# Kernel tuning notes

Hardware: AMD Instinct MI355X
Metric: run time of the kernel (lower is better)

Reference implementation:

```python
import jax, jax.numpy as jnp
import numpy as np

B, S, FEAT, HID, H = 8, 1024, 1024, 1024, 8
DH = HID // H  # head dim = 128
MASK_VAL = -128.0  # mask_val = -2**7 (soft additive mask, per original code)


def setup_inputs() -> dict:
    key = jax.random.key(0)
    ks = jax.random.split(key, 4)
    scale = 0.02
    return {
        "queries": jax.random.normal(ks[0], (B, S, FEAT), dtype=jnp.float32),
        "Wq": jax.random.normal(ks[1], (FEAT, HID), dtype=jnp.float32) * scale,
        "bq": jnp.zeros((HID,), dtype=jnp.float32),
        "Wk": jax.random.normal(ks[2], (FEAT, HID), dtype=jnp.float32) * scale,
        "bk": jnp.zeros((HID,), dtype=jnp.float32),
        "Wv": jax.random.normal(ks[3], (FEAT, HID), dtype=jnp.float32) * scale,
        "bv": jnp.zeros((HID,), dtype=jnp.float32),
    }


def reference(queries, Wq, bq, Wk, bk, Wv, bv):
    # Self-attention: keys = values = queries (torch forward defaults)
    q = queries @ Wq + bq  # [B,S,HID]
    k = queries @ Wk + bk
    v = queries @ Wv + bv
    # split heads: chunk along last dim == reshape (B,S,H,DH)
    qh = q.reshape(B, S, H, DH)
    kh = k.reshape(B, S, H, DH)
    vh = v.reshape(B, S, H, DH)
    # exp-scaled-dot score (non-standard: exp BEFORE mask/softmax)
    logits = jnp.einsum("bqhd,bkhd->bhqk", qh, kh) / np.float32(np.sqrt(DH))
    score = jnp.exp(logits)
    # soft additive causal mask: upper triangle (diag=1) gets -128
    mask = jnp.triu(jnp.full((S, S), MASK_VAL, dtype=score.dtype), k=1)
    att = jax.nn.softmax(score + mask, axis=-1)  # [B,H,S,S]
    ctx = jnp.einsum("bhqk,bkhd->bqhd", att, vh)  # [B,S,H,DH]
    # reverse heads: concat along last dim
    return ctx.reshape(B, S, HID)
```

## Files before the change

kernel.cpp:

```cpp
#include <hip/hip_runtime.h>


typedef __bf16 bf16x8 __attribute__((ext_vector_type(8)));
typedef float floatx4 __attribute__((ext_vector_type(4)));
typedef unsigned short u16;
typedef unsigned int u32;

#define RSCALE 0.08838834764831845f

__device__ __forceinline__ u16 f2b(float f) {
  union { float f; unsigned u; } v; v.f = f;
  return (u16)((v.u + 0x7FFFu + ((v.u >> 16) & 1u)) >> 16);
}

__device__ __forceinline__ void gld_lds16(const void* g, void* l) {
  __builtin_amdgcn_global_load_lds(
      (const __attribute__((address_space(1))) unsigned*)g,
      (__attribute__((address_space(3))) unsigned*)l, 16, 0, 0);
}

#define MFMA16(a, b, c) __builtin_amdgcn_mfma_f32_16x16x32_bf16(a, b, c, 0, 0, 0)

__device__ __forceinline__ void barrier_mem() {
  asm volatile("" ::: "memory");
  __builtin_amdgcn_s_barrier();
  asm volatile("" ::: "memory");
}
#define WAIT_LGKM0() asm volatile("s_waitcnt lgkmcnt(0)" ::: "memory")
#define WAIT_VM4()   asm volatile("s_waitcnt vmcnt(4)" ::: "memory")
#define WAIT_VM0()   asm volatile("s_waitcnt vmcnt(0)" ::: "memory")

__global__ __launch_bounds__(256) void prep_kernel(
    const float4* __restrict__ X, u16* __restrict__ Xb,
    const float* __restrict__ Wq, const float* __restrict__ Wk,
    const float* __restrict__ Wv, u16* __restrict__ Wtb) {
  if (blockIdx.x < 8192) {
    unsigned i = blockIdx.x * 256u + threadIdx.x;
    float4 v = X[i];
    ushort4 o;
    o.x = f2b(v.x); o.y = f2b(v.y); o.z = f2b(v.z); o.w = f2b(v.w);
    *reinterpret_cast<ushort4*>(Xb + 4u * i) = o;
  } else {
    const int bid = blockIdx.x - 8192;
    const int mat = bid >> 10;
    const int bx = bid & 31, by = (bid >> 5) & 31;
    const float* W = (mat == 0) ? Wq : (mat == 1) ? Wk : Wv;
    u16* Wt = Wtb + (size_t)mat * (1024u * 1024u);
    __shared__ u16 tile[32][33];
    const int x = threadIdx.x & 31, y = threadIdx.x >> 5;
    const int kt = bx * 32, nt = by * 32;
#pragma unroll
    for (int i = 0; i < 4; ++i)
      tile[y + 8 * i][x] = f2b(W[(size_t)(kt + y + 8 * i) * 1024 + nt + x]);
    __syncthreads();
#pragma unroll
    for (int i = 0; i < 4; ++i)
      Wt[(size_t)(nt + y + 8 * i) * 1024 + kt + x] = tile[x][y + 8 * i];
  }
}

__global__ __launch_bounds__(512, 2) void gemm_qkv_kernel(
    const u16* __restrict__ Xb, const u16* __restrict__ Wtb,
    const float* __restrict__ bq, const float* __restrict__ bk,
    const float* __restrict__ bv, u16* __restrict__ Qh, u16* __restrict__ Kh,
    u16* __restrict__ Vt) {
  const int id = blockIdx.x;
  const int swz = (id & 7) * 48 + (id >> 3);
  const int m0 = (swz / 12) * 256;
  const int n0g = (swz % 12) * 256;

  __shared__ u16 As[2][256 * 64];
  __shared__ u16 Bs[2][256 * 64];

  const int tid = threadIdx.x;
  const int wid = tid >> 6;
  const int lane = tid & 63;
  const int quad = lane >> 4;
  const int l16 = lane & 15;
  const int swzr = l16 & 7;
  const int wrm = (wid >> 2) * 128;
  const int wcn = (wid & 3) * 64;

  const int srow = tid >> 3;
  const int sunit = (tid & 7) ^ (srow & 7);

  auto stageA = [&](int buf, int h, int kk) {
#pragma unroll
    for (int c = 0; c < 2; ++c)
      gld_lds16(
          Xb + (size_t)(m0 + h * 128 + c * 64 + srow) * 1024 + kk + sunit * 8,
          &As[buf][(h * 128 + c * 64 + wid * 8) * 64]);
  };
  auto stageB = [&](int buf, int h, int kk) {
#pragma unroll
    for (int c = 0; c < 2; ++c)
      gld_lds16(
          Wtb + (size_t)(n0g + h * 128 + c * 64 + srow) * 1024 + kk + sunit * 8,
          &Bs[buf][(h * 128 + c * 64 + wid * 8) * 64]);
  };

  const floatx4 z4 = {0.f, 0.f, 0.f, 0.f};
  floatx4 acc[8][4];
#pragma unroll
  for (int i = 0; i < 8; ++i)
#pragma unroll
    for (int j = 0; j < 4; ++j) acc[i][j] = z4;

  bf16x8 aR[4][2];
  bf16x8 bA[2][2];
  bf16x8 bB[2][2];

  stageA(0, 0, 0); stageA(0, 1, 0);
  stageB(0, 0, 0); stageB(0, 1, 0);
  stageB(1, 0, 64); stageB(1, 1, 64);
  WAIT_VM4();
  barrier_mem();

#pragma unroll 1
  for (int t = 0; t < 16; ++t) {
    const u16* __restrict__ Ab = As[t & 1];
    const u16* __restrict__ Bb = Bs[t & 1];
    const int nb = (t + 1) & 1;

#pragma unroll
    for (int i = 0; i < 4; ++i)
#pragma unroll
      for (int c = 0; c < 2; ++c)
        aR[i][c] = *(const bf16x8*)(Ab + (wrm + i * 16 + l16) * 64 +
                                    (((c * 4 + quad) ^ swzr) * 8));
#pragma unroll
    for (int j = 0; j < 2; ++j)
#pragma unroll
      for (int c = 0; c < 2; ++c)
        bA[j][c] = *(const bf16x8*)(Bb + (wcn + j * 16 + l16) * 64 +
                                    (((c * 4 + quad) ^ swzr) * 8));
    if (t < 15) stageA(nb, 0, (t + 1) * 64);
    barrier_mem();
    WAIT_LGKM0();
    __builtin_amdgcn_s_setprio(1);
#pragma unroll
    for (int c = 0; c < 2; ++c)
#pragma unroll
      for (int i = 0; i < 4; ++i)
#pragma unroll
        for (int j = 0; j < 2; ++j)
          acc[i][j] = MFMA16(aR[i][c], bA[j][c], acc[i][j]);
    __builtin_amdgcn_s_setprio(0);
    barrier_mem();

#pragma unroll
    for (int j = 0; j < 2; ++j)
#pragma unroll
      for (int c = 0; c < 2; ++c)
        bB[j][c] = *(const bf16x8*)(Bb + (wcn + 32 + j * 16 + l16) * 64 +
                                    (((c * 4 + quad) ^ swzr) * 8));
    if (t < 15) stageA(nb, 1, (t + 1) * 64);
    barrier_mem();
    WAIT_LGKM0();
    __builtin_amdgcn_s_setprio(1);
#pragma unroll
    for (int c = 0; c < 2; ++c)
#pragma unroll
      for (int i = 0; i < 4; ++i)
#pragma unroll
        for (int j = 0; j < 2; ++j)
          acc[i][2 + j] = MFMA16(aR[i][c], bB[j][c], acc[i][2 + j]);
    __builtin_amdgcn_s_setprio(0);
    barrier_mem();

#pragma unroll
    for (int i = 0; i < 4; ++i)
#pragma unroll
      for (int c = 0; c < 2; ++c)
        aR[i][c] = *(const bf16x8*)(Ab + (wrm + 64 + i * 16 + l16) * 64 +
                                    (((c * 4 + quad) ^ swzr) * 8));
    if (t < 14) stageB(t & 1, 0, (t + 2) * 64);
    barrier_mem();
    WAIT_LGKM0();
    __builtin_amdgcn_s_setprio(1);
#pragma unroll
    for (int c = 0; c < 2; ++c)
#pragma unroll
      for (int i = 0; i < 4; ++i)
#pragma unroll
        for (int j = 0; j < 2; ++j)
          acc[4 + i][2 + j] = MFMA16(aR[i][c], bB[j][c], acc[4 + i][2 + j]);
    __builtin_amdgcn_s_setprio(0);
    barrier_mem();

    if (t < 14) stageB(t & 1, 1, (t + 2) * 64);
    barrier_mem();
    WAIT_LGKM0();
    __builtin_amdgcn_s_setprio(1);
#pragma unroll
    for (int c = 0; c < 2; ++c)
#pragma unroll
      for (int i = 0; i < 4; ++i)
#pragma unroll
        for (int j = 0; j < 2; ++j)
          acc[4 + i][j] = MFMA16(aR[i][c], bA[j][c], acc[4 + i][j]);
    __builtin_amdgcn_s_setprio(0);
    if (t < 14) { WAIT_VM4(); }
    else if (t == 14) { WAIT_VM0(); }
    barrier_mem();
  }

  const int mat = n0g >> 10;
  const int nn = n0g & 1023;
  const float* __restrict__ bias = (mat == 0) ? bq : (mat == 1) ? bk : bv;
  const int b = m0 >> 10;
  const int sbase = (m0 & 1023) + wrm;
  float bias4[4];
#pragma unroll
  for (int j = 0; j < 4; ++j) bias4[j] = bias[nn + wcn + j * 16 + l16];

  if (mat < 2) {
    u16* outp = (mat == 0 ? Qh : Kh) + (size_t)b * 8 * 1024 * 128;
#pragma unroll
    for (int fi = 0; fi < 8; ++fi)
#pragma unroll
      for (int j = 0; j < 4; ++j) {
        const int dg = nn + wcn + j * 16 + l16;
        const int h = dg >> 7, d = dg & 127;
        const int s = sbase + fi * 16 + quad * 4;
        u16* p = outp + (size_t)h * 1024 * 128 + (size_t)s * 128 + d;
#pragma unroll
        for (int r = 0; r < 4; ++r)
          p[(size_t)r * 128] = f2b(acc[fi][j][r] + bias4[j]);
      }
  } else {
    u16* outp = Vt + (size_t)b * 8 * 128 * 1024;
#pragma unroll
    for (int fi = 0; fi < 8; ++fi)
#pragma unroll
      for (int j = 0; j < 4; ++j) {
        const int dg = nn + wcn + j * 16 + l16;
        const int h = dg >> 7, d = dg & 127;
        const int s = sbase + fi * 16 + quad * 4;
        ushort4 pk;
        pk.x = f2b(acc[fi][j][0] + bias4[j]);
        pk.y = f2b(acc[fi][j][1] + bias4[j]);
        pk.z = f2b(acc[fi][j][2] + bias4[j]);
        pk.w = f2b(acc[fi][j][3] + bias4[j]);
        *(ushort4*)(outp + (size_t)h * 128 * 1024 + (size_t)d * 1024 + s) = pk;
      }
  }
}

__global__ __launch_bounds__(256, 2) void attn_kernel(const u16* __restrict__ Qh,
                                                      const u16* __restrict__ Kh,
                                                      const u16* __restrict__ Vt,
                                                      float* __restrict__ out) {
  const int id = blockIdx.x;
  const int x = id & 7;
  const int j = id >> 3;
  const int bh = x * 8 + (j & 7);
  const int QTMAP[8] = {7, 5, 6, 4, 0, 2, 1, 3};
  const int qt = QTMAP[j >> 3];
  const int q0 = qt * 128;

  const int tid = threadIdx.x;
  const int wid = tid >> 6;
  const int lane = tid & 63;
  const int quad = lane >> 4;
  const int l16 = lane & 15;

  __shared__ u16 Ks[2][64 * 128];
  __shared__ u16 Vs[2][128 * 64];
  __shared__ u16 Ps[4][32 * 32];

  const u16* __restrict__ Qbase = Qh + (size_t)bh * 1024 * 128;
  const u16* __restrict__ Kbase = Kh + (size_t)bh * 1024 * 128;
  const u16* __restrict__ Vbase = Vt + (size_t)bh * 128 * 1024;

  const int qw = q0 + wid * 32;

  bf16x8 qf[2][4];
#pragma unroll
  for (int nt = 0; nt < 2; ++nt)
#pragma unroll
    for (int c = 0; c < 4; ++c)
      qf[nt][c] = *(const bf16x8*)(Qbase + (size_t)(qw + nt * 16 + l16) * 128 +
                                   c * 32 + quad * 8);

  const floatx4 z4 = {0.f, 0.f, 0.f, 0.f};
  floatx4 o[2][8];
#pragma unroll
  for (int nt = 0; nt < 2; ++nt)
#pragma unroll
    for (int dt = 0; dt < 8; ++dt) o[nt][dt] = z4;
  float lacc[2] = {0.f, 0.f};

  auto stage = [&](int b, int k0) {
#pragma unroll
    for (int c = 0; c < 4; ++c) {
      const int r0 = wid * 16 + c * 4;
      const int row = r0 + quad;
      gld_lds16(Kbase + (size_t)(k0 + row) * 128 + ((l16 ^ (c * 4 + quad)) * 8),
                Ks[b] + r0 * 128);
    }
#pragma unroll
    for (int c = 0; c < 4; ++c) {
      const int r0 = wid * 32 + c * 8;
      const int row = r0 + (lane >> 3);
      gld_lds16(Vbase + (size_t)row * 1024 + k0 +
                    (((lane & 7) ^ ((lane >> 3) & 7)) * 8),
                Vs[b] + r0 * 64);
    }
  };

  const int n = (q0 + 128) >> 6;
  stage(0, 0);

  for (int i = 0; i < n; ++i) {
    const int k0 = i << 6;
    __syncthreads();
    if (i + 1 < n) stage((i + 1) & 1, k0 + 64);

    const u16* __restrict__ Kb = Ks[i & 1];
    const u16* __restrict__ Vb = Vs[i & 1];

#pragma unroll
    for (int half = 0; half < 2; ++half) {
      if (k0 + half * 32 > qw + 31) break;

#pragma unroll
      for (int f2 = 0; f2 < 2; ++f2) {
        const int f = half * 2 + f2;
        bf16x8 kf[4];
#pragma unroll
        for (int c = 0; c < 4; ++c)
          kf[c] = *(const bf16x8*)(Kb + (f * 16 + l16) * 128 +
                                   (((c * 4 + quad) ^ l16) * 8));
        floatx4 st[2];
#pragma unroll
        for (int nt = 0; nt < 2; ++nt) {
          st[nt] = z4;
#pragma unroll
          for (int c = 0; c < 4; ++c) st[nt] = MFMA16(kf[c], qf[nt][c], st[nt]);
        }
        const int kb = k0 + f * 16 + quad * 4;
#pragma unroll
        for (int nt = 0; nt < 2; ++nt) {
          const int qrow = qw + nt * 16 + l16;
          float p[4];
#pragma unroll
          for (int r = 0; r < 4; ++r) {
            const float e = fminf(__expf(st[nt][r] * RSCALE), 85.f);
            p[r] = (kb + r > qrow) ? 0.f : __expf(e);
          }
          lacc[nt] += (p[0] + p[1]) + (p[2] + p[3]);
          uint2 pk;
          pk.x = (u32)f2b(p[0]) | ((u32)f2b(p[1]) << 16);
          pk.y = (u32)f2b(p[2]) | ((u32)f2b(p[3]) << 16);
          *(uint2*)((char*)Ps[wid] + (nt * 16 + l16) * 64 +
                    (((f2 * 2 + (quad >> 1)) ^ (l16 & 3)) * 16) +
                    (quad & 1) * 8) = pk;
        }
      }
      asm volatile("s_waitcnt lgkmcnt(0)" ::: "memory");

      bf16x8 pa[2];
#pragma unroll
      for (int nt = 0; nt < 2; ++nt)
        pa[nt] = *(const bf16x8*)((char*)Ps[wid] + (nt * 16 + l16) * 64 +
                                  ((quad ^ (l16 & 3)) * 16));
#pragma unroll
      for (int dt = 0; dt < 8; ++dt) {
        const bf16x8 vf = *(const bf16x8*)(
            Vb + (dt * 16 + l16) * 64 +
            (((half * 4 + quad) ^ (l16 & 7)) * 8));
        o[0][dt] = MFMA16(vf, pa[0], o[0][dt]);
        o[1][dt] = MFMA16(vf, pa[1], o[1][dt]);
      }
    }
  }

  float linv[2];
#pragma unroll
  for (int nt = 0; nt < 2; ++nt) {
    float s = lacc[nt];
    s += __shfl_xor(s, 16);
    s += __shfl_xor(s, 32);
    linv[nt] = 1.0f / s;
  }

  float* outp = out + (size_t)(bh >> 3) * 1024 * 1024 + (bh & 7) * 128;
#pragma unroll
  for (int nt = 0; nt < 2; ++nt) {
    const int qrow = qw + nt * 16 + l16;
#pragma unroll
    for (int dt = 0; dt < 8; ++dt) {
      float4 v;
      v.x = o[nt][dt][0] * linv[nt];
      v.y = o[nt][dt][1] * linv[nt];
      v.z = o[nt][dt][2] * linv[nt];
      v.w = o[nt][dt][3] * linv[nt];
      *(float4*)(outp + (size_t)qrow * 1024 + dt * 16 + quad * 4) = v;
    }
  }
}

extern "C" void kernel_launch(void* const* d_in, const int* in_sizes, int n_in,
                              void* d_out, int out_size, void* d_ws,
                              size_t ws_size, hipStream_t stream) {
  const float* X = (const float*)d_in[0];
  const float* Wq = (const float*)d_in[1];
  const float* bq = (const float*)d_in[2];
  const float* Wk = (const float*)d_in[3];
  const float* bk = (const float*)d_in[4];
  const float* Wv = (const float*)d_in[5];
  const float* bv = (const float*)d_in[6];
  float* out = (float*)d_out;

  char* ws = (char*)d_ws;
  u16* Xb  = (u16*)(ws);
  u16* Wtb = (u16*)(ws + (16u << 20));
  u16* Qh  = (u16*)(ws + (22u << 20));
  u16* Kh  = (u16*)(ws + (38u << 20));
  u16* Vt  = (u16*)(ws + (54u << 20));

  prep_kernel<<<8192 + 3072, 256, 0, stream>>>((const float4*)X, Xb, Wq, Wk,
                                               Wv, Wtb);
  gemm_qkv_kernel<<<384, 512, 0, stream>>>(Xb, Wtb, bq, bk, bv, Qh, Kh, Vt);
  attn_kernel<<<512, 256, 0, stream>>>(Qh, Kh, Vt, out);
}
```

Baseline: 206.9 us.

## Reorder projection GEMM main loop into K-half phases with full B-tile reuse

The QKV projection GEMM inner loop is restructured. Each phase now loads one K-half (32 elements) for all four B column tiles and two A row groups, instead of splitting by column half. The staging of the second B half moves one iteration later, so the wait threshold drops from vmcnt(4) to vmcnt(2). The barrier helper with memory clobbers is replaced by bare s_barrier and waitcnt asm, which reduces compiler fences. This risks the compiler reordering LDS accesses across barriers.

```diff
diff --git a/kernel.cpp b/kernel.cpp
--- a/kernel.cpp
+++ b/kernel.cpp
@@ -20,15 +20,6 @@
 }
 
 #define MFMA16(a, b, c) __builtin_amdgcn_mfma_f32_16x16x32_bf16(a, b, c, 0, 0, 0)
-
-__device__ __forceinline__ void barrier_mem() {
-  asm volatile("" ::: "memory");
-  __builtin_amdgcn_s_barrier();
-  asm volatile("" ::: "memory");
-}
-#define WAIT_LGKM0() asm volatile("s_waitcnt lgkmcnt(0)" ::: "memory")
-#define WAIT_VM4()   asm volatile("s_waitcnt vmcnt(4)" ::: "memory")
-#define WAIT_VM0()   asm volatile("s_waitcnt vmcnt(0)" ::: "memory")
 
 __global__ __launch_bounds__(256) void prep_kernel(
     const float4* __restrict__ X, u16* __restrict__ Xb,
@@ -106,15 +97,13 @@
 #pragma unroll
     for (int j = 0; j < 4; ++j) acc[i][j] = z4;
 
-  bf16x8 aR[4][2];
-  bf16x8 bA[2][2];
-  bf16x8 bB[2][2];
+  bf16x8 a0[4], a1[4], bR[4];
 
   stageA(0, 0, 0); stageA(0, 1, 0);
   stageB(0, 0, 0); stageB(0, 1, 0);
   stageB(1, 0, 64); stageB(1, 1, 64);
-  WAIT_VM4();
-  barrier_mem();
+  asm volatile("s_waitcnt vmcnt(4)");
+  __builtin_amdgcn_s_barrier();
 
 #pragma unroll 1
   for (int t = 0; t < 16; ++t) {
@@ -124,85 +113,82 @@
 
 #pragma unroll
     for (int i = 0; i < 4; ++i)
-#pragma unroll
-      for (int c = 0; c < 2; ++c)
-        aR[i][c] = *(const bf16x8*)(Ab + (wrm + i * 16 + l16) * 64 +
-                                    (((c * 4 + quad) ^ swzr) * 8));
-#pragma unroll
-    for (int j = 0; j < 2; ++j)
-#pragma unroll
-      for (int c = 0; c < 2; ++c)
-        bA[j][c] = *(const bf16x8*)(Bb + (wcn + j * 16 + l16) * 64 +
-                                    (((c * 4 + quad) ^ swzr) * 8));
-    if (t < 15) stageA(nb, 0, (t + 1) * 64);
-    barrier_mem();
-    WAIT_LGKM0();
+      a0[i] = *(const bf16x8*)(Ab + (wrm + i * 16 + l16) * 64 +
+                               ((quad ^ swzr) * 8));
+#pragma unroll
+    for (int j = 0; j < 4; ++j)
+      bR[j] = *(const bf16x8*)(Bb + (wcn + j * 16 + l16) * 64 +
+                               ((quad ^ swzr) * 8));
+    if (t < 15) {
+      stageA(nb, 0, (t + 1) * 64);
+      if (t >= 1) stageB(nb, 1, (t + 1) * 64);
+    }
+    __builtin_amdgcn_s_barrier();
+    asm volatile("s_waitcnt lgkmcnt(0)");
     __builtin_amdgcn_s_setprio(1);
 #pragma unroll
-    for (int c = 0; c < 2; ++c)
-#pragma unroll
-      for (int i = 0; i < 4; ++i)
-#pragma unroll
-        for (int j = 0; j < 2; ++j)
-          acc[i][j] = MFMA16(aR[i][c], bA[j][c], acc[i][j]);
+    for (int i = 0; i < 4; ++i)
+#pragma unroll
+      for (int j = 0; j < 4; ++j)
+        acc[i][j] = MFMA16(a0[i], bR[j], acc[i][j]);
     __builtin_amdgcn_s_setprio(0);
-    barrier_mem();
-
-#pragma unroll
-    for (int j = 0; j < 2; ++j)
-#pragma unroll
-      for (int c = 0; c < 2; ++c)
-        bB[j][c] = *(const bf16x8*)(Bb + (wcn + 32 + j * 16 + l16) * 64 +
-                                    (((c * 4 + quad) ^ swzr) * 8));
+    __builtin_amdgcn_s_barrier();
+
+#pragma unroll
+    for (int i = 0; i < 4; ++i)
+      a1[i] = *(const bf16x8*)(Ab + (wrm + 64 + i * 16 + l16) * 64 +
+                               ((quad ^ swzr) * 8));
     if (t < 15) stageA(nb, 1, (t + 1) * 64);
-    barrier_mem();
-    WAIT_LGKM0();
+    __builtin_amdgcn_s_barrier();
+    asm volatile("s_waitcnt lgkmcnt(0)");
     __builtin_amdgcn_s_setprio(1);
 #pragma unroll
-    for (int c = 0; c < 2; ++c)
-#pragma unroll
-      for (int i = 0; i < 4; ++i)
-#pragma unroll
-        for (int j = 0; j < 2; ++j)
-          acc[i][2 + j] = MFMA16(aR[i][c], bB[j][c], acc[i][2 + j]);
+    for (int i = 0; i < 4; ++i)
+#pragma unroll
+      for (int j = 0; j < 4; ++j)
+        acc[4 + i][j] = MFMA16(a1[i], bR[j], acc[4 + i][j]);
     __builtin_amdgcn_s_setprio(0);
-    barrier_mem();
-
-#pragma unroll
-    for (int i = 0; i < 4; ++i)
-#pragma unroll
-      for (int c = 0; c < 2; ++c)
-        aR[i][c] = *(const bf16x8*)(Ab + (wrm + 64 + i * 16 + l16) * 64 +
-                                    (((c * 4 + quad) ^ swzr) * 8));
+    __builtin_amdgcn_s_barrier();
+
+#pragma unroll
+    for (int i = 0; i < 4; ++i)
+      a0[i] = *(const bf16x8*)(Ab + (wrm + i * 16 + l16) * 64 +
+                               (((4 + quad) ^ swzr) * 8));
+#pragma unroll
+    for (int j = 0; j < 4; ++j)
+      bR[j] = *(const bf16x8*)(Bb + (wcn + j * 16 + l16) * 64 +
+                               (((4 + quad) ^ swzr) * 8));
+    __builtin_amdgcn_s_barrier();
+    asm volatile("s_waitcnt lgkmcnt(0)");
+    __builtin_amdgcn_s_setprio(1);
+#pragma unroll
+    for (int i = 0; i < 4; ++i)
+#pragma unroll
+      for (int j = 0; j < 4; ++j)
+        acc[i][j] = MFMA16(a0[i], bR[j], acc[i][j]);
+    __builtin_amdgcn_s_setprio(0);
+    __builtin_amdgcn_s_barrier();
+
+#pragma unroll
+    for (int i = 0; i < 4; ++i)
+      a1[i] = *(const bf16x8*)(Ab + (wrm + 64 + i * 16 + l16) * 64 +
+                               (((4 + quad) ^ swzr) * 8));
     if (t < 14) stageB(t & 1, 0, (t + 2) * 64);
-    barrier_mem();
-    WAIT_LGKM0();
+    __builtin_amdgcn_s_barrier();
+    asm volatile("s_waitcnt lgkmcnt(0)");
     __builtin_amdgcn_s_setprio(1);
 #pragma unroll
-    for (int c = 0; c < 2; ++c)
-#pragma unroll
-      for (int i = 0; i < 4; ++i)
-#pragma unroll
-        for (int j = 0; j < 2; ++j)
-          acc[4 + i][2 + j] = MFMA16(aR[i][c], bB[j][c], acc[4 + i][2 + j]);
+    for (int i = 0; i < 4; ++i)
+#pragma unroll
+      for (int j = 0; j < 4; ++j)
+        acc[4 + i][j] = MFMA16(a1[i], bR[j], acc[4 + i][j]);
     __builtin_amdgcn_s_setprio(0);
-    barrier_mem();
-
-    if (t < 14) stageB(t & 1, 1, (t + 2) * 64);
-    barrier_mem();
-    WAIT_LGKM0();
-    __builtin_amdgcn_s_setprio(1);
-#pragma unroll
-    for (int c = 0; c < 2; ++c)
-#pragma unroll
-      for (int i = 0; i < 4; ++i)
-#pragma unroll
-        for (int j = 0; j < 2; ++j)
-          acc[4 + i][j] = MFMA16(aR[i][c], bA[j][c], acc[4 + i][j]);
-    __builtin_amdgcn_s_setprio(0);
-    if (t < 14) { WAIT_VM4(); }
-    else if (t == 14) { WAIT_VM0(); }
-    barrier_mem();
+    if (t < 14) {
+      asm volatile("s_waitcnt vmcnt(2)");
+    } else if (t == 14) {
+      asm volatile("s_waitcnt vmcnt(0)");
+    }
+    __builtin_amdgcn_s_barrier();
   }
 
   const int mat = n0g >> 10;
```

Result: no change. 207.9 us (+0.5%).
